# Kernel tuning notes

Measured on AMD Instinct MI355X. Metric: run time of the kernel, lower is better.

## Reference

```python
import jax, jax.numpy as jnp
import numpy as np

B, T, C, H, L, V = 4, 1024, 1024, 16, 6, 32000
D = C // H
STD = 0.02


def setup_inputs() -> dict:
    key = jax.random.key(0)
    ks = jax.random.split(key, 12)
    return {
        "idx": jax.random.randint(ks[0], (B, T), 0, V),
        "tok_emb": jax.random.normal(ks[1], (V, C), jnp.float32) * STD,
        "pos_emb": jax.random.normal(ks[2], (T, C), jnp.float32) * STD,
        "qkv_w": jax.random.normal(ks[3], (L, C, 3 * C), jnp.float32) * STD,
        "attn_out_w": jax.random.normal(ks[4], (L, C, C), jnp.float32) * STD,
        "attn_out_b": jnp.zeros((L, C), jnp.float32),
        "fc1_w": jax.random.normal(ks[5], (L, C, 4 * C), jnp.float32) * STD,
        "fc1_b": jnp.zeros((L, 4 * C), jnp.float32),
        "fc2_w": jax.random.normal(ks[6], (L, 4 * C, C), jnp.float32) * STD,
        "fc2_b": jnp.zeros((L, C), jnp.float32),
        "ln1_w": jnp.ones((L, C), jnp.float32),
        "ln1_b": jnp.zeros((L, C), jnp.float32),
        "ln2_w": jnp.ones((L, C), jnp.float32),
        "ln2_b": jnp.zeros((L, C), jnp.float32),
        "lnf_w": jnp.ones((C,), jnp.float32),
        "lnf_b": jnp.zeros((C,), jnp.float32),
        "head_w": jax.random.normal(ks[7], (C, V), jnp.float32) * STD,
    }


def layernorm(x, w, b, eps=1e-5):
    mu = jnp.mean(x, axis=-1, keepdims=True)
    var = jnp.var(x, axis=-1, keepdims=True)
    return (x - mu) * jax.lax.rsqrt(var + eps) * w + b


def attention(x, qkv_w, out_w, out_b, causal_mask):
    # x: (B,T,C)
    qkv = jnp.einsum("btc,cf->btf", x, qkv_w)  # (B,T,3C)
    q, k, v = jnp.split(qkv, 3, axis=-1)
    q = q.reshape(B, T, H, D).transpose(0, 2, 1, 3)  # (B,H,T,D)
    k = k.reshape(B, T, H, D).transpose(0, 2, 1, 3)
    v = v.reshape(B, T, H, D).transpose(0, 2, 1, 3)
    scores = jnp.einsum("bhqd,bhkd->bhqk", q, k) / np.sqrt(D).astype(np.float32)
    scores = jnp.where(causal_mask, scores, -jnp.inf)
    w = jax.nn.softmax(scores, axis=-1)
    out = jnp.einsum("bhqk,bhkd->bhqd", w, v)  # (B,H,T,D)
    out = out.transpose(0, 2, 1, 3).reshape(B, T, C)
    return jnp.einsum("btc,cd->btd", out, out_w) + out_b


def reference(idx, tok_emb, pos_emb, qkv_w, attn_out_w, attn_out_b,
              fc1_w, fc1_b, fc2_w, fc2_b, ln1_w, ln1_b, ln2_w, ln2_b,
              lnf_w, lnf_b, head_w):
    causal_mask = jnp.tril(jnp.ones((T, T), dtype=bool))[None, None]  # (1,1,T,T)
    x = tok_emb[idx] + pos_emb[jnp.arange(T)][None]  # (B,T,C)
    for l in range(L):
        h = layernorm(x, ln1_w[l], ln1_b[l])
        x = x + attention(h, qkv_w[l], attn_out_w[l], attn_out_b[l], causal_mask)
        h = layernorm(x, ln2_w[l], ln2_b[l])
        h = jax.nn.relu(jnp.einsum("btc,cf->btf", h, fc1_w[l]) + fc1_b[l])
        x = x + jnp.einsum("btf,fc->btc", h, fc2_w[l]) + fc2_b[l]
    x = layernorm(x, lnf_w, lnf_b)
    logits = jnp.einsum("btc,cv->btv", x, head_w)  # (B,T,V)
    return logits
```

## Files before the change

kernel.cpp:

```cpp
#include <hip/hip_runtime.h>
#include <cstdint>
#include <cstddef>

typedef __bf16 bf16_t;
typedef __bf16 bf16x8 __attribute__((ext_vector_type(8)));
typedef float f32x4 __attribute__((ext_vector_type(4)));
typedef int i32x4 __attribute__((ext_vector_type(4)));
typedef short short4v __attribute__((ext_vector_type(4)));

#define B_ 4
#define T_ 1024
#define C_ 1024
#define H_ 16
#define L_ 6
#define V_ 32000
#define M_ (B_ * T_)

__global__ __launch_bounds__(256) void k_embed(const int* __restrict__ idx,
                                               const float* __restrict__ tok,
                                               const float* __restrict__ pos,
                                               float* __restrict__ x) {
  int row = blockIdx.x;
  int t = row & (T_ - 1);
  int id = idx[row];
  int c = threadIdx.x * 4;
  f32x4 a = *(const f32x4*)(tok + (size_t)id * C_ + c);
  f32x4 p = *(const f32x4*)(pos + (size_t)t * C_ + c);
  *(f32x4*)(x + (size_t)row * C_ + c) = a + p;
}

__global__ __launch_bounds__(256) void k_ln(const float* __restrict__ x,
                                            const float* __restrict__ w,
                                            const float* __restrict__ b,
                                            bf16_t* __restrict__ out) {
  __shared__ float red[8];
  int row = blockIdx.x;
  int tid = threadIdx.x;
  const float* xr = x + (size_t)row * C_;
  f32x4 v = *(const f32x4*)(xr + tid * 4);
  float s = v[0] + v[1] + v[2] + v[3];
  float q = v[0] * v[0] + v[1] * v[1] + v[2] * v[2] + v[3] * v[3];
#pragma unroll
  for (int off = 32; off; off >>= 1) {
    s += __shfl_xor(s, off);
    q += __shfl_xor(q, off);
  }
  int wid = tid >> 6;
  if ((tid & 63) == 0) { red[wid * 2] = s; red[wid * 2 + 1] = q; }
  __syncthreads();
  s = red[0] + red[2] + red[4] + red[6];
  q = red[1] + red[3] + red[5] + red[7];
  float mu = s * (1.f / C_);
  float var = q * (1.f / C_) - mu * mu;
  float rstd = rsqrtf(var + 1e-5f);
  f32x4 wv = *(const f32x4*)(w + tid * 4);
  f32x4 bv = *(const f32x4*)(b + tid * 4);
  bf16_t* o = out + (size_t)row * C_ + tid * 4;
#pragma unroll
  for (int j = 0; j < 4; j++) o[j] = (bf16_t)((v[j] - mu) * rstd * wv[j] + bv[j]);
}

__global__ __launch_bounds__(256) void k_transpose_bf16(const float* __restrict__ in,
                                                        bf16_t* __restrict__ out,
                                                        int K, int N) {
  __shared__ float tile[32][33];
  int n0 = blockIdx.x * 32, k0 = blockIdx.y * 32;
  int tid = threadIdx.x;
  int cr = tid >> 5, cc = tid & 31;
#pragma unroll
  for (int it = 0; it < 4; it++) {
    int r = it * 8 + cr;
    tile[r][cc] = in[(size_t)(k0 + r) * N + n0 + cc];
  }
  __syncthreads();
#pragma unroll
  for (int it = 0; it < 4; it++) {
    int r = it * 8 + cr;
    out[(size_t)(n0 + r) * K + k0 + cc] = (bf16_t)tile[cc][r];
  }
}

__global__ __launch_bounds__(256) void k_transpose_layer(
    const float* __restrict__ qkvw, const float* __restrict__ attnw,
    const float* __restrict__ fc1w, const float* __restrict__ fc2w,
    bf16_t* __restrict__ qkvT, bf16_t* __restrict__ owT,
    bf16_t* __restrict__ fc1T, bf16_t* __restrict__ fc2T) {
  __shared__ float tile[32][33];
  int tb = blockIdx.x;
  const float* in;
  bf16_t* out;
  int K, N;
  bool qs = false;
  if (tb < 3072) { in = qkvw; out = qkvT; K = 1024; N = 3072; qs = true; }
  else if (tb < 4096) { tb -= 3072; in = attnw; out = owT; K = 1024; N = 1024; }
  else if (tb < 8192) { tb -= 4096; in = fc1w; out = fc1T; K = 1024; N = 4096; }
  else { tb -= 8192; in = fc2w; out = fc2T; K = 4096; N = 1024; }
  int nTx = N >> 5;
  int n0 = (tb % nTx) * 32, k0 = (tb / nTx) * 32;
  int tid = threadIdx.x;
  int cr = tid >> 5, cc = tid & 31;
#pragma unroll
  for (int it = 0; it < 4; it++) {
    int r = it * 8 + cr;
    tile[r][cc] = in[(size_t)(k0 + r) * N + n0 + cc];
  }
  __syncthreads();
#pragma unroll
  for (int it = 0; it < 4; it++) {
    int r = it * 8 + cr;
    float v = tile[cc][r];
    if (qs && (n0 + r) < 1024) v *= 0.125f;
    out[(size_t)(n0 + r) * K + k0 + cc] = (bf16_t)v;
  }
}

__global__ __launch_bounds__(256) void k_attn(const bf16_t* __restrict__ qh,
                                              const bf16_t* __restrict__ kh,
                                              const bf16_t* __restrict__ vT,
                                              bf16_t* __restrict__ outb) {
  __shared__ bf16_t p_lds[4][16 * 72];
  int tid = threadIdx.x, lane = tid & 63, wid = tid >> 6;
  int bh = blockIdx.x;
  int b = bh >> 4, h = bh & (H_ - 1);
  int qbase = blockIdx.y * 64 + wid * 16;
  const bf16_t* qp = qh + ((size_t)bh * T_ + qbase) * 64;
  const bf16_t* kp = kh + (size_t)bh * T_ * 64;
  const bf16_t* vp = vT + (size_t)bh * 64 * T_;
  int r = lane & 15, g = lane >> 4;

  bf16x8 qf0 = *(const bf16x8*)(qp + r * 64 + g * 8);
  bf16x8 qf1 = *(const bf16x8*)(qp + r * 64 + 32 + g * 8);

  f32x4 o[4];
  float m[4], l[4];
#pragma unroll
  for (int j = 0; j < 4; j++) { m[j] = -1e30f; l[j] = 0.f; o[j] = (f32x4){0.f, 0.f, 0.f, 0.f}; }

  int kv_end = qbase + 16;
  for (int jb = 0; jb < kv_end; jb += 64) {
    f32x4 s[4];
#pragma unroll
    for (int t = 0; t < 4; t++) s[t] = (f32x4){0.f, 0.f, 0.f, 0.f};
    const bf16_t* kb = kp + (size_t)(jb + r) * 64 + g * 8;
#pragma unroll
    for (int t = 0; t < 4; t++) {
      const bf16_t* kt = kb + (size_t)t * 16 * 64;
      s[t] = __builtin_amdgcn_mfma_f32_16x16x32_bf16(qf0, *(const bf16x8*)(kt), s[t], 0, 0, 0);
      s[t] = __builtin_amdgcn_mfma_f32_16x16x32_bf16(qf1, *(const bf16x8*)(kt + 32), s[t], 0, 0, 0);
    }

    bool needMask = (jb + 63 > qbase);
    float pv[4][4], fac[4];
#pragma unroll
    for (int j = 0; j < 4; j++) {
      int rowg = qbase + g * 4 + j;
      float v0 = s[0][j], v1 = s[1][j], v2 = s[2][j], v3 = s[3][j];
      if (needMask) {
        if (jb + r > rowg) v0 = -1e30f;
        if (jb + 16 + r > rowg) v1 = -1e30f;
        if (jb + 32 + r > rowg) v2 = -1e30f;
        if (jb + 48 + r > rowg) v3 = -1e30f;
      }
      float t0 = fmaxf(fmaxf(v0, v1), fmaxf(v2, v3));
      t0 = fmaxf(t0, __shfl_xor(t0, 1));
      t0 = fmaxf(t0, __shfl_xor(t0, 2));
      t0 = fmaxf(t0, __shfl_xor(t0, 4));
      t0 = fmaxf(t0, __shfl_xor(t0, 8));
      float nm = fmaxf(m[j], t0);
      pv[j][0] = __expf(v0 - nm);
      pv[j][1] = __expf(v1 - nm);
      pv[j][2] = __expf(v2 - nm);
      pv[j][3] = __expf(v3 - nm);
      float f = __expf(m[j] - nm);
      float ts = (pv[j][0] + pv[j][1]) + (pv[j][2] + pv[j][3]);
      ts += __shfl_xor(ts, 1);
      ts += __shfl_xor(ts, 2);
      ts += __shfl_xor(ts, 4);
      ts += __shfl_xor(ts, 8);
      l[j] = l[j] * f + ts;
      m[j] = nm;
      fac[j] = f;
    }
    f32x4 fv = (f32x4){fac[0], fac[1], fac[2], fac[3]};
#pragma unroll
    for (int d = 0; d < 4; d++) o[d] *= fv;

    bf16_t* pl = p_lds[wid];
#pragma unroll
    for (int j = 0; j < 4; j++)
#pragma unroll
      for (int t = 0; t < 4; t++)
        pl[(g * 4 + j) * 72 + t * 16 + r] = (bf16_t)pv[j][t];

    bf16x8 pa0 = *(const bf16x8*)(pl + r * 72 + g * 8);
    bf16x8 pa1 = *(const bf16x8*)(pl + r * 72 + 32 + g * 8);
#pragma unroll
    for (int d = 0; d < 4; d++) {
      const bf16_t* vf = vp + (size_t)(d * 16 + r) * T_ + jb + g * 8;
      o[d] = __builtin_amdgcn_mfma_f32_16x16x32_bf16(pa0, *(const bf16x8*)(vf), o[d], 0, 0, 0);
      o[d] = __builtin_amdgcn_mfma_f32_16x16x32_bf16(pa1, *(const bf16x8*)(vf + 32), o[d], 0, 0, 0);
    }
  }

#pragma unroll
  for (int d = 0; d < 4; d++) {
#pragma unroll
    for (int j = 0; j < 4; j++) {
      float val = o[d][j] / l[j];
      outb[((size_t)(b * T_ + qbase + g * 4 + j)) * C_ + h * 64 + d * 16 + r] = (bf16_t)val;
    }
  }
}

__device__ __forceinline__ void gld_lds16(const bf16_t* g, bf16_t* l) {
  __builtin_amdgcn_global_load_lds((const __attribute__((address_space(1))) void*)g,
                                   (__attribute__((address_space(3))) void*)l, 16, 0, 0);
}
__device__ __forceinline__ bf16x8 lds_rd128(uint32_t addr) {
  i32x4 d;
  asm volatile("ds_read_b128 %0, %1" : "=v"(d) : "v"(addr));
  return __builtin_bit_cast(bf16x8, d);
}
#define BAR_() __builtin_amdgcn_s_barrier()
#define SCHED0_() __builtin_amdgcn_sched_barrier(0)
#define WLGN_(n)                                                           \
  do {                                                                     \
    asm volatile("s_waitcnt lgkmcnt(" #n ")" ::: "memory");                \
    SCHED0_();                                                             \
  } while (0)

template <int MODE, int HASB, int HASRELU, int HASRES>
__global__ __launch_bounds__(256, 2) void k_gemm(const bf16_t* __restrict__ A,
                                                 const bf16_t* __restrict__ Bt,
                                                 const float* __restrict__ bias,
                                                 const float* resid,
                                                 void* Cout, int M, int N, int K) {
  __shared__ bf16_t As[2][128][64];
  __shared__ bf16_t Bs[2][128][64];
  bf16_t* AsF = &As[0][0][0];
  bf16_t* BsF = &Bs[0][0][0];
  const uint32_t asb = (uint32_t)(uintptr_t)AsF;
  const uint32_t bsb = (uint32_t)(uintptr_t)BsF;

  int tid = threadIdx.x, lane = tid & 63, w = tid >> 6;
  int wr = w >> 1, wc = w & 1;
  int r15 = lane & 15, g4 = lane >> 4;

  int nwg = (int)(gridDim.x * gridDim.y);
  int bid = (int)(blockIdx.y * gridDim.x + blockIdx.x);
  int xcd = bid & 7, loc = bid >> 3;
  int q8 = nwg >> 3, r8 = nwg & 7;
  int swz = (xcd < r8) ? xcd * (q8 + 1) + loc : r8 * (q8 + 1) + (xcd - r8) * q8 + loc;
  int nY = M >> 7;
  int by = swz % nY, bx = swz / nY;
  size_t rowBase = (size_t)by * 128;
  size_t colBase = (size_t)bx * 128;

  int srowL = (lane >> 3);
  int scol = ((lane & 7) ^ srowL) * 8;

  uint32_t xm = (uint32_t)((r15 & 7) << 4);
  uint32_t offK0 = ((uint32_t)(g4 * 16)) ^ xm;
  uint32_t offK1 = ((uint32_t)(g4 * 16 + 64)) ^ xm;
  uint32_t aRd = asb + (uint32_t)((wr * 64 + r15) * 128);
  uint32_t bRd = bsb + (uint32_t)((wc * 64 + r15) * 128);

  f32x4 acc[4][4];
#pragma unroll
  for (int i = 0; i < 4; i++)
#pragma unroll
    for (int j = 0; j < 4; j++) acc[i][j] = (f32x4){0.f, 0.f, 0.f, 0.f};

  bf16x8 a0[4], a1[4], b0[4], b1[4];

#define KSTAGE_(tk, bufv)                                                            \
  do {                                                                               \
    _Pragma("unroll") for (int _q = 0; _q < 4; _q++) {                               \
      int _row = _q * 32 + w * 8 + srowL;                                            \
      const bf16_t* _ga = A + (rowBase + _row) * (size_t)K + (size_t)(tk)*64 + scol; \
      const bf16_t* _gb = Bt + (colBase + _row) * (size_t)K + (size_t)(tk)*64 + scol;\
      gld_lds16(_ga, AsF + (bufv)*8192 + _q * 2048 + w * 512);                       \
      gld_lds16(_gb, BsF + (bufv)*8192 + _q * 2048 + w * 512);                       \
    }                                                                                \
  } while (0)

#define KRDS_(aset, bset, kk, bufv)                                                  \
  do {                                                                               \
    uint32_t _off = (kk) ? offK1 : offK0;                                            \
    uint32_t _ab = aRd + (uint32_t)(bufv)*16384u + _off;                             \
    uint32_t _bb = bRd + (uint32_t)(bufv)*16384u + _off;                             \
    _Pragma("unroll") for (int _m = 0; _m < 4; _m++)                                 \
        aset[_m] = lds_rd128(_ab + _m * 2048);                                       \
    _Pragma("unroll") for (int _n = 0; _n < 4; _n++)                                 \
        bset[_n] = lds_rd128(_bb + _n * 2048);                                       \
  } while (0)

#define KMFH_(aset, bset)                                                            \
  do {                                                                               \
    __builtin_amdgcn_s_setprio(1);                                                   \
    _Pragma("unroll") for (int _m = 0; _m < 4; _m++)                                 \
        _Pragma("unroll") for (int _n = 0; _n < 4; _n++)                             \
            acc[_m][_n] = __builtin_amdgcn_mfma_f32_16x16x32_bf16(                   \
                aset[_m], bset[_n], acc[_m][_n], 0, 0, 0);                           \
    __builtin_amdgcn_s_setprio(0);                                                   \
  } while (0)

  KSTAGE_(0, 0);
  asm volatile("s_waitcnt vmcnt(0)" ::: "memory");
  BAR_();

  int NT = K >> 6;
  for (int kt = 0; kt < NT; ++kt) {
    int buf = kt & 1;
    bool pf = (kt + 1 < NT);
    if (pf) KSTAGE_(kt + 1, buf ^ 1);
    KRDS_(a0, b0, 0, buf);
    KRDS_(a1, b1, 1, buf);
    WLGN_(8);
    KMFH_(a0, b0);
    WLGN_(0);
    KMFH_(a1, b1);
    asm volatile("s_waitcnt vmcnt(0)" ::: "memory");
    BAR_();
  }

#pragma unroll
  for (int i = 0; i < 4; i++) {
    size_t row0 = rowBase + wr * 64 + i * 16 + g4 * 4;
#pragma unroll
    for (int j = 0; j < 4; j++) {
      size_t col = colBase + wc * 64 + j * 16 + r15;
      float bi = HASB ? bias[col] : 0.f;
      if (MODE == 2) {
        float vv[4];
#pragma unroll
        for (int q = 0; q < 4; q++) vv[q] = acc[i][j][q];
        int part = (int)(col >> 10);
        int within = (int)col & 1023;
        int hh = within >> 6, dd = within & 63;
        int bb = (int)(row0 >> 10), tt = (int)row0 & 1023;
        size_t bhh = (size_t)(bb * 16 + hh);
        if (part < 2) {
          bf16_t* dstp = (bf16_t*)Cout + (size_t)part * ((size_t)M_ * C_);
#pragma unroll
          for (int q = 0; q < 4; q++)
            dstp[(bhh * 1024 + tt + q) * 64 + dd] = (bf16_t)vv[q];
        } else {
          bf16_t* dstp = (bf16_t*)Cout + 2 * ((size_t)M_ * C_);
          short4v pk;
#pragma unroll
          for (int q = 0; q < 4; q++) {
            bf16_t bv = (bf16_t)vv[q];
            pk[q] = __builtin_bit_cast(short, bv);
          }
          *(short4v*)(dstp + (bhh * 64 + dd) * 1024 + tt) = pk;
        }
      } else {
#pragma unroll
        for (int q = 0; q < 4; q++) {
          size_t row = row0 + q;
          float v = acc[i][j][q] + bi;
          if (HASRELU) v = fmaxf(v, 0.f);
          if (HASRES) v += resid[row * (size_t)N + col];
          if (MODE == 1)
            ((bf16_t*)Cout)[row * (size_t)N + col] = (bf16_t)v;
          else
            ((float*)Cout)[row * (size_t)N + col] = v;
        }
      }
    }
  }
#undef KSTAGE_
#undef KRDS_
#undef KMFH_
}

#define STAGE_(q, tk, bufv)                                                           \
  do {                                                                                \
    const bf16_t* _ga = A + (size_t)(rowBase + (q)*64 + srow) * (size_t)K +           \
                        (size_t)(tk)*64 + scol;                                       \
    const bf16_t* _gb = Bt + (size_t)(colBase + (q)*64 + srow) * (size_t)K +          \
                        (size_t)(tk)*64 + scol;                                       \
    gld_lds16(_ga, AsF + (bufv)*16384 + (q)*4096 + w * 512);                          \
    gld_lds16(_gb, BsF + (bufv)*16384 + (q)*4096 + w * 512);                          \
  } while (0)

#define RDS_(aset, bset, kk, bufv)                                                    \
  do {                                                                                \
    uint32_t _off = (kk) ? offK1 : offK0;                                             \
    uint32_t _ab = aRd + (uint32_t)(bufv)*32768u + _off;                              \
    uint32_t _bb = bRd + (uint32_t)(bufv)*32768u + _off;                              \
    _Pragma("unroll") for (int _m = 0; _m < 8; _m++)                                  \
        aset[_m] = lds_rd128(_ab + _m * 2048);                                        \
    _Pragma("unroll") for (int _n = 0; _n < 4; _n++)                                  \
        bset[_n] = lds_rd128(_bb + _n * 2048);                                        \
  } while (0)

#define MFH_(aset, bset)                                                              \
  do {                                                                                \
    __builtin_amdgcn_s_setprio(1);                                                    \
    _Pragma("unroll") for (int _m = 0; _m < 8; _m++)                                  \
        _Pragma("unroll") for (int _n = 0; _n < 4; _n++)                              \
            acc[_m][_n] = __builtin_amdgcn_mfma_f32_16x16x32_bf16(                    \
                aset[_m], bset[_n], acc[_m][_n], 0, 0, 0);                            \
    __builtin_amdgcn_s_setprio(0);                                                    \
  } while (0)

template <int OUTBF, int HASB, int HASRELU, int HASRES>
__global__ __launch_bounds__(512, 2) void k_gemm256(const bf16_t* __restrict__ A,
                                                    const bf16_t* __restrict__ Bt,
                                                    const float* __restrict__ bias,
                                                    const float* resid,
                                                    void* Cout, int M, int N, int K) {
  __shared__ bf16_t As[2][256][64];
  __shared__ bf16_t Bs[2][256][64];
  bf16_t* AsF = &As[0][0][0];
  bf16_t* BsF = &Bs[0][0][0];
  const uint32_t asb = (uint32_t)(uintptr_t)AsF;
  const uint32_t bsb = (uint32_t)(uintptr_t)BsF;

  int tid = threadIdx.x, lane = tid & 63, w = tid >> 6;
  int wr = w >> 2, wc = w & 3;
  int r15 = lane & 15, g4 = lane >> 4;

  int nwg = (int)gridDim.x;
  int bid = (int)blockIdx.x;
  int xcd = bid & 7, loc = bid >> 3;
  int q8 = nwg >> 3, r8 = nwg & 7;
  int swz = (xcd < r8) ? xcd * (q8 + 1) + loc : r8 * (q8 + 1) + (xcd - r8) * q8 + loc;
  int nY = M >> 8;
  int by = swz % nY, bx = swz / nY;
  int rowBase = by * 256, colBase = bx * 256;

  int srow = w * 8 + (lane >> 3);
  int scol = ((lane & 7) ^ (lane >> 3)) * 8;

  uint32_t xm = (uint32_t)((r15 & 7) << 4);
  uint32_t offK0 = ((uint32_t)(g4 * 16)) ^ xm;
  uint32_t offK1 = ((uint32_t)(g4 * 16 + 64)) ^ xm;
  uint32_t aRd = asb + (uint32_t)((wr * 128 + r15) * 128);
  uint32_t bRd = bsb + (uint32_t)((wc * 64 + r15) * 128);

  f32x4 acc[8][4];
#pragma unroll
  for (int i = 0; i < 8; i++)
#pragma unroll
    for (int j = 0; j < 4; j++) acc[i][j] = (f32x4){0.f, 0.f, 0.f, 0.f};

  bf16x8 a0[8], a1[8], b0[4], b1[4];

#pragma unroll
  for (int q = 0; q < 4; q++) STAGE_(q, 0, 0);
  asm volatile("s_waitcnt vmcnt(0)" ::: "memory");
  BAR_();

  int NT = K >> 6;
  for (int kt = 0; kt < NT; ++kt) {
    int buf = kt & 1;
    bool pf = (kt + 1 < NT);
    if (pf) {
#pragma unroll
      for (int q = 0; q < 4; q++) STAGE_(q, kt + 1, buf ^ 1);
    }
    RDS_(a0, b0, 0, buf);
    RDS_(a1, b1, 1, buf);
    WLGN_(12);
    MFH_(a0, b0);
    WLGN_(0);
    MFH_(a1, b1);
    asm volatile("s_waitcnt vmcnt(0)" ::: "memory");
    BAR_();
  }

#pragma unroll
  for (int m = 0; m < 8; m++) {
    size_t row0 = (size_t)rowBase + wr * 128 + m * 16 + g4 * 4;
#pragma unroll
    for (int n = 0; n < 4; n++) {
      size_t col = (size_t)colBase + wc * 64 + n * 16 + r15;
      float bi = HASB ? bias[col] : 0.f;
#pragma unroll
      for (int qq = 0; qq < 4; qq++) {
        size_t row = row0 + qq;
        float v = acc[m][n][qq] + bi;
        if (HASRELU) v = fmaxf(v, 0.f);
        if (HASRES) v += resid[row * (size_t)N + col];
        if (OUTBF)
          ((bf16_t*)Cout)[row * (size_t)N + col] = (bf16_t)v;
        else
          ((float*)Cout)[row * (size_t)N + col] = v;
      }
    }
  }
}

extern "C" void kernel_launch(void* const* d_in, const int* in_sizes, int n_in,
                              void* d_out, int out_size, void* d_ws, size_t ws_size,
                              hipStream_t stream) {
  (void)in_sizes; (void)n_in; (void)out_size; (void)ws_size;
  const int* idx = (const int*)d_in[0];
  const float* tok_emb = (const float*)d_in[1];
  const float* pos_emb = (const float*)d_in[2];
  const float* qkv_w = (const float*)d_in[3];
  const float* attn_out_w = (const float*)d_in[4];
  const float* attn_out_b = (const float*)d_in[5];
  const float* fc1_w = (const float*)d_in[6];
  const float* fc1_b = (const float*)d_in[7];
  const float* fc2_w = (const float*)d_in[8];
  const float* fc2_b = (const float*)d_in[9];
  const float* ln1_w = (const float*)d_in[10];
  const float* ln1_b = (const float*)d_in[11];
  const float* ln2_w = (const float*)d_in[12];
  const float* ln2_b = (const float*)d_in[13];
  const float* lnf_w = (const float*)d_in[14];
  const float* lnf_b = (const float*)d_in[15];
  const float* head_w = (const float*)d_in[16];
  float* out = (float*)d_out;

  char* wsp = (char*)d_ws;
  auto alloc = [&](size_t bytes) {
    char* p = wsp;
    wsp += (bytes + 255) & ~(size_t)255;
    return p;
  };
  float* x      = (float*)alloc((size_t)M_ * C_ * 4);
  bf16_t* hbuf  = (bf16_t*)alloc((size_t)M_ * C_ * 2);
  bf16_t* qhb   = (bf16_t*)alloc((size_t)3 * M_ * C_ * 2);
  bf16_t* khb   = qhb + (size_t)M_ * C_;
  bf16_t* vTb   = khb + (size_t)M_ * C_;
  bf16_t* attnb = (bf16_t*)alloc((size_t)M_ * C_ * 2);
  bf16_t* midb  = (bf16_t*)alloc((size_t)M_ * 4 * C_ * 2);
  bf16_t* qkvwT = (bf16_t*)alloc((size_t)3 * C_ * C_ * 2);
  bf16_t* owT   = (bf16_t*)alloc((size_t)C_ * C_ * 2);
  bf16_t* fc1wT = (bf16_t*)alloc((size_t)4 * C_ * C_ * 2);
  bf16_t* fc2wT = (bf16_t*)alloc((size_t)4 * C_ * C_ * 2);
  bf16_t* headwT= (bf16_t*)alloc((size_t)C_ * V_ * 2);

  k_embed<<<M_, 256, 0, stream>>>(idx, tok_emb, pos_emb, x);
  k_transpose_bf16<<<dim3(V_ / 32, C_ / 32), 256, 0, stream>>>(head_w, headwT, C_, V_);

  for (int l = 0; l < L_; l++) {
    k_transpose_layer<<<12288, 256, 0, stream>>>(
        qkv_w + (size_t)l * C_ * 3 * C_, attn_out_w + (size_t)l * C_ * C_,
        fc1_w + (size_t)l * C_ * 4 * C_, fc2_w + (size_t)l * 4 * C_ * C_,
        qkvwT, owT, fc1wT, fc2wT);

    k_ln<<<M_, 256, 0, stream>>>(x, ln1_w + l * C_, ln1_b + l * C_, hbuf);
    k_gemm<2, 0, 0, 0><<<dim3(3 * C_ / 128, M_ / 128), 256, 0, stream>>>(
        hbuf, qkvwT, nullptr, nullptr, qhb, M_, 3 * C_, C_);
    k_attn<<<dim3(B_ * H_, T_ / 64), 256, 0, stream>>>(qhb, khb, vTb, attnb);
    k_gemm<0, 1, 0, 1><<<dim3(C_ / 128, M_ / 128), 256, 0, stream>>>(
        attnb, owT, attn_out_b + l * C_, x, x, M_, C_, C_);

    k_ln<<<M_, 256, 0, stream>>>(x, ln2_w + l * C_, ln2_b + l * C_, hbuf);
    k_gemm<1, 1, 1, 0><<<dim3(4 * C_ / 128, M_ / 128), 256, 0, stream>>>(
        hbuf, fc1wT, fc1_b + (size_t)l * 4 * C_, nullptr, midb, M_, 4 * C_, C_);
    k_gemm<0, 1, 0, 1><<<dim3(C_ / 128, M_ / 128), 256, 0, stream>>>(
        midb, fc2wT, fc2_b + l * C_, x, x, M_, C_, 4 * C_);
  }

  k_ln<<<M_, 256, 0, stream>>>(x, lnf_w, lnf_b, hbuf);
  k_gemm256<0, 0, 0, 0><<<dim3((V_ / 256) * (M_ / 256)), 512, 0, stream>>>(
      hbuf, headwT, nullptr, nullptr, out, M_, V_, C_);
}
```

Baseline: 2.063 ms.

## Transpose V in a separate kernel and use 128-tile GEMM for head

The QKV GEMM epilogue no longer writes V directly in transposed layout. It now writes V in the same head-major layout as Q and K, and a new LDS-tiled kernel k_vtrans transposes it into a separate buffer before attention. The specialized 256x256 head GEMM kernel is also removed, and the vocabulary projection now uses the generic 128-tile k_gemm. This simplifies the code but adds an extra kernel launch and V memory traffic per layer, and it likely loses the efficiency of the larger-tile head GEMM.

```diff
diff --git a/kernel.cpp b/kernel.cpp
--- a/kernel.cpp
+++ b/kernel.cpp
@@ -6,7 +6,6 @@
 typedef __bf16 bf16x8 __attribute__((ext_vector_type(8)));
 typedef float f32x4 __attribute__((ext_vector_type(4)));
 typedef int i32x4 __attribute__((ext_vector_type(4)));
-typedef short short4v __attribute__((ext_vector_type(4)));
 
 #define B_ 4
 #define T_ 1024
@@ -111,6 +110,28 @@
     float v = tile[cc][r];
     if (qs && (n0 + r) < 1024) v *= 0.125f;
     out[(size_t)(n0 + r) * K + k0 + cc] = (bf16_t)v;
+  }
+}
+
+__global__ __launch_bounds__(256) void k_vtrans(const bf16_t* __restrict__ vh,
+                                                bf16_t* __restrict__ vT) {
+  __shared__ bf16_t tile[64][65];
+  int bh = blockIdx.x;
+  int t0 = blockIdx.y * 64;
+  int tid = threadIdx.x;
+  int c = tid & 63, rr = tid >> 6;
+  const bf16_t* src = vh + ((size_t)bh * T_ + t0) * 64;
+#pragma unroll
+  for (int it = 0; it < 16; it++) {
+    int r = it * 4 + rr;
+    tile[r][c] = src[(size_t)r * 64 + c];
+  }
+  __syncthreads();
+  bf16_t* dst = vT + (size_t)bh * 64 * T_ + t0;
+#pragma unroll
+  for (int it = 0; it < 16; it++) {
+    int dr = it * 4 + rr;
+    dst[(size_t)dr * T_ + c] = tile[c][dr];
   }
 }
 
@@ -332,29 +353,15 @@
       size_t col = colBase + wc * 64 + j * 16 + r15;
       float bi = HASB ? bias[col] : 0.f;
       if (MODE == 2) {
-        float vv[4];
-#pragma unroll
-        for (int q = 0; q < 4; q++) vv[q] = acc[i][j][q];
         int part = (int)(col >> 10);
         int within = (int)col & 1023;
         int hh = within >> 6, dd = within & 63;
         int bb = (int)(row0 >> 10), tt = (int)row0 & 1023;
         size_t bhh = (size_t)(bb * 16 + hh);
-        if (part < 2) {
-          bf16_t* dstp = (bf16_t*)Cout + (size_t)part * ((size_t)M_ * C_);
-#pragma unroll
-          for (int q = 0; q < 4; q++)
-            dstp[(bhh * 1024 + tt + q) * 64 + dd] = (bf16_t)vv[q];
-        } else {
-          bf16_t* dstp = (bf16_t*)Cout + 2 * ((size_t)M_ * C_);
-          short4v pk;
-#pragma unroll
-          for (int q = 0; q < 4; q++) {
-            bf16_t bv = (bf16_t)vv[q];
-            pk[q] = __builtin_bit_cast(short, bv);
-          }
-          *(short4v*)(dstp + (bhh * 64 + dd) * 1024 + tt) = pk;
-        }
+        bf16_t* dstp = (bf16_t*)Cout + (size_t)part * ((size_t)M_ * C_);
+#pragma unroll
+        for (int q = 0; q < 4; q++)
+          dstp[(bhh * 1024 + tt + q) * 64 + dd] = (bf16_t)acc[i][j][q];
       } else {
 #pragma unroll
         for (int q = 0; q < 4; q++) {
@@ -373,125 +380,6 @@
 #undef KSTAGE_
 #undef KRDS_
 #undef KMFH_
-}
-
-#define STAGE_(q, tk, bufv)                                                           \
-  do {                                                                                \
-    const bf16_t* _ga = A + (size_t)(rowBase + (q)*64 + srow) * (size_t)K +           \
-                        (size_t)(tk)*64 + scol;                                       \
-    const bf16_t* _gb = Bt + (size_t)(colBase + (q)*64 + srow) * (size_t)K +          \
-                        (size_t)(tk)*64 + scol;                                       \
-    gld_lds16(_ga, AsF + (bufv)*16384 + (q)*4096 + w * 512);                          \
-    gld_lds16(_gb, BsF + (bufv)*16384 + (q)*4096 + w * 512);                          \
-  } while (0)
-
-#define RDS_(aset, bset, kk, bufv)                                                    \
-  do {                                                                                \
-    uint32_t _off = (kk) ? offK1 : offK0;                                             \
-    uint32_t _ab = aRd + (uint32_t)(bufv)*32768u + _off;                              \
-    uint32_t _bb = bRd + (uint32_t)(bufv)*32768u + _off;                              \
-    _Pragma("unroll") for (int _m = 0; _m < 8; _m++)                                  \
-        aset[_m] = lds_rd128(_ab + _m * 2048);                                        \
-    _Pragma("unroll") for (int _n = 0; _n < 4; _n++)                                  \
-        bset[_n] = lds_rd128(_bb + _n * 2048);                                        \
-  } while (0)
-
-#define MFH_(aset, bset)                                                              \
-  do {                                                                                \
-    __builtin_amdgcn_s_setprio(1);                                                    \
-    _Pragma("unroll") for (int _m = 0; _m < 8; _m++)                                  \
-        _Pragma("unroll") for (int _n = 0; _n < 4; _n++)                              \
-            acc[_m][_n] = __builtin_amdgcn_mfma_f32_16x16x32_bf16(                    \
-                aset[_m], bset[_n], acc[_m][_n], 0, 0, 0);                            \
-    __builtin_amdgcn_s_setprio(0);                                                    \
-  } while (0)
-
-template <int OUTBF, int HASB, int HASRELU, int HASRES>
-__global__ __launch_bounds__(512, 2) void k_gemm256(const bf16_t* __restrict__ A,
-                                                    const bf16_t* __restrict__ Bt,
-                                                    const float* __restrict__ bias,
-                                                    const float* resid,
-                                                    void* Cout, int M, int N, int K) {
-  __shared__ bf16_t As[2][256][64];
-  __shared__ bf16_t Bs[2][256][64];
-  bf16_t* AsF = &As[0][0][0];
-  bf16_t* BsF = &Bs[0][0][0];
-  const uint32_t asb = (uint32_t)(uintptr_t)AsF;
-  const uint32_t bsb = (uint32_t)(uintptr_t)BsF;
-
-  int tid = threadIdx.x, lane = tid & 63, w = tid >> 6;
-  int wr = w >> 2, wc = w & 3;
-  int r15 = lane & 15, g4 = lane >> 4;
-
-  int nwg = (int)gridDim.x;
-  int bid = (int)blockIdx.x;
-  int xcd = bid & 7, loc = bid >> 3;
-  int q8 = nwg >> 3, r8 = nwg & 7;
-  int swz = (xcd < r8) ? xcd * (q8 + 1) + loc : r8 * (q8 + 1) + (xcd - r8) * q8 + loc;
-  int nY = M >> 8;
-  int by = swz % nY, bx = swz / nY;
-  int rowBase = by * 256, colBase = bx * 256;
-
-  int srow = w * 8 + (lane >> 3);
-  int scol = ((lane & 7) ^ (lane >> 3)) * 8;
-
-  uint32_t xm = (uint32_t)((r15 & 7) << 4);
-  uint32_t offK0 = ((uint32_t)(g4 * 16)) ^ xm;
-  uint32_t offK1 = ((uint32_t)(g4 * 16 + 64)) ^ xm;
-  uint32_t aRd = asb + (uint32_t)((wr * 128 + r15) * 128);
-  uint32_t bRd = bsb + (uint32_t)((wc * 64 + r15) * 128);
-
-  f32x4 acc[8][4];
-#pragma unroll
-  for (int i = 0; i < 8; i++)
-#pragma unroll
-    for (int j = 0; j < 4; j++) acc[i][j] = (f32x4){0.f, 0.f, 0.f, 0.f};
-
-  bf16x8 a0[8], a1[8], b0[4], b1[4];
-
-#pragma unroll
-  for (int q = 0; q < 4; q++) STAGE_(q, 0, 0);
-  asm volatile("s_waitcnt vmcnt(0)" ::: "memory");
-  BAR_();
-
-  int NT = K >> 6;
-  for (int kt = 0; kt < NT; ++kt) {
-    int buf = kt & 1;
-    bool pf = (kt + 1 < NT);
-    if (pf) {
-#pragma unroll
-      for (int q = 0; q < 4; q++) STAGE_(q, kt + 1, buf ^ 1);
-    }
-    RDS_(a0, b0, 0, buf);
-    RDS_(a1, b1, 1, buf);
-    WLGN_(12);
-    MFH_(a0, b0);
-    WLGN_(0);
-    MFH_(a1, b1);
-    asm volatile("s_waitcnt vmcnt(0)" ::: "memory");
-    BAR_();
-  }
-
-#pragma unroll
-  for (int m = 0; m < 8; m++) {
-    size_t row0 = (size_t)rowBase + wr * 128 + m * 16 + g4 * 4;
-#pragma unroll
-    for (int n = 0; n < 4; n++) {
-      size_t col = (size_t)colBase + wc * 64 + n * 16 + r15;
-      float bi = HASB ? bias[col] : 0.f;
-#pragma unroll
-      for (int qq = 0; qq < 4; qq++) {
-        size_t row = row0 + qq;
-        float v = acc[m][n][qq] + bi;
-        if (HASRELU) v = fmaxf(v, 0.f);
-        if (HASRES) v += resid[row * (size_t)N + col];
-        if (OUTBF)
-          ((bf16_t*)Cout)[row * (size_t)N + col] = (bf16_t)v;
-        else
-          ((float*)Cout)[row * (size_t)N + col] = v;
-      }
-    }
-  }
 }
 
 extern "C" void kernel_launch(void* const* d_in, const int* in_sizes, int n_in,
@@ -527,7 +415,8 @@
   bf16_t* hbuf  = (bf16_t*)alloc((size_t)M_ * C_ * 2);
   bf16_t* qhb   = (bf16_t*)alloc((size_t)3 * M_ * C_ * 2);
   bf16_t* khb   = qhb + (size_t)M_ * C_;
-  bf16_t* vTb   = khb + (size_t)M_ * C_;
+  bf16_t* vhb   = khb + (size_t)M_ * C_;
+  bf16_t* vTb   = (bf16_t*)alloc((size_t)M_ * C_ * 2);
   bf16_t* attnb = (bf16_t*)alloc((size_t)M_ * C_ * 2);
   bf16_t* midb  = (bf16_t*)alloc((size_t)M_ * 4 * C_ * 2);
   bf16_t* qkvwT = (bf16_t*)alloc((size_t)3 * C_ * C_ * 2);
@@ -548,6 +437,7 @@
     k_ln<<<M_, 256, 0, stream>>>(x, ln1_w + l * C_, ln1_b + l * C_, hbuf);
     k_gemm<2, 0, 0, 0><<<dim3(3 * C_ / 128, M_ / 128), 256, 0, stream>>>(
         hbuf, qkvwT, nullptr, nullptr, qhb, M_, 3 * C_, C_);
+    k_vtrans<<<dim3(B_ * H_, T_ / 64), 256, 0, stream>>>(vhb, vTb);
     k_attn<<<dim3(B_ * H_, T_ / 64), 256, 0, stream>>>(qhb, khb, vTb, attnb);
     k_gemm<0, 1, 0, 1><<<dim3(C_ / 128, M_ / 128), 256, 0, stream>>>(
         attnb, owT, attn_out_b + l * C_, x, x, M_, C_, C_);
@@ -560,6 +450,6 @@
   }
 
   k_ln<<<M_, 256, 0, stream>>>(x, lnf_w, lnf_b, hbuf);
-  k_gemm256<0, 0, 0, 0><<<dim3((V_ / 256) * (M_ / 256)), 512, 0, stream>>>(
+  k_gemm<0, 0, 0, 0><<<dim3(V_ / 128, M_ / 128), 256, 0, stream>>>(
       hbuf, headwT, nullptr, nullptr, out, M_, V_, C_);
 }
```

After: 2.149 ms. 4.2% more time.
